# Kernel tuning notes

Hardware: AMD Instinct MI355X
Metric: run time of the kernel (lower is better)

## Reference

```python
import jax, jax.numpy as jnp
import numpy as np

LOG2E = 1.44269504


def setup_inputs() -> dict:
    key = jax.random.key(0)
    k1, k2, k3, k4 = jax.random.split(key, 4)
    B, Sq, Skv, Hq, Hkv, D = 2, 2048, 2048, 16, 4, 128
    q = jax.random.normal(k1, (B, Sq, Hq, D), dtype=jnp.float32)
    k = jax.random.normal(k2, (B, Skv, Hkv, D), dtype=jnp.float32)
    v = jax.random.normal(k3, (B, Skv, Hkv, D), dtype=jnp.float32)
    attn_mask = jax.random.normal(k4, (B, Hq, Sq, Skv), dtype=jnp.float32)
    return {"q": q, "k": k, "v": v, "attn_mask": attn_mask}


def reference(q, k, v, attn_mask):
    # q: [B, Sq, Hq, D]; k, v: [B, Skv, Hkv, D]; attn_mask: [B, Hq, Sq, Skv]
    B, Sq, Hq, D = q.shape
    Skv, Hkv = k.shape[1], k.shape[2]
    sm_scale = 1.0 / (D ** 0.5)

    qt = jnp.transpose(q, (0, 2, 1, 3))  # [B, Hq, Sq, D]
    kt = jnp.transpose(k, (0, 2, 1, 3))  # [B, Hkv, Skv, D]
    vt = jnp.transpose(v, (0, 2, 1, 3))  # [B, Hkv, Skv, D]

    # GQA head sharing: q-head h reads kv-head h % Hkv
    head_map = jnp.arange(Hq) % Hkv
    ke = kt[:, head_map]  # [B, Hq, Skv, D]
    ve = vt[:, head_map]  # [B, Hq, Skv, D]

    # scaled scores + additive mask (kernel: qk*sm_scale + attn_mask)
    logits = jnp.einsum('bhqd,bhkd->bhqk', qt, ke) * sm_scale + attn_mask

    # causal masking: kernel adds -1e6 in the log2 domain after LOG2E scaling
    s2 = logits * LOG2E
    causal_ok = jnp.arange(Sq)[:, None] >= jnp.arange(Skv)[None, :]
    s2 = s2 + jnp.where(causal_ok, 0.0, -1000000.0)

    # online-softmax equivalent: stable exp2 softmax along kv
    m = jnp.max(s2, axis=-1, keepdims=True)
    p = jnp.exp2(s2 - m)  # [B, Hq, Sq, Skv]
    l = jnp.sum(p, axis=-1, keepdims=True)
    o = jnp.einsum('bhqk,bhkd->bhqd', p, ve) / l

    return jnp.transpose(o, (0, 2, 1, 3))  # [B, Sq, Hq, D]
```

## Files before the change

kernel.cpp:

```cpp
#include <hip/hip_runtime.h>
#include <hip/hip_bf16.h>
#include <stdint.h>

static constexpr int B_   = 2;
static constexpr int SQ   = 2048;
static constexpr int SKV  = 2048;
static constexpr int HQ   = 16;
static constexpr int HKV  = 4;
static constexpr int DH   = 128;

static constexpr int BM = 64;
static constexpr int BN = 64;

static constexpr int KLD = DH + 8;
static constexpr int VLD = BN + 6;
static constexpr int PLD = BN + 4;

#define LOG2E 1.44269504f
static constexpr float SM_SCALE = 0.08838834764831845f;

static constexpr float SMAX = 24.0f;

typedef unsigned short ushort_t;
typedef __attribute__((ext_vector_type(8))) short bf16x8;
typedef __attribute__((ext_vector_type(4))) short bf16x4;
typedef __attribute__((ext_vector_type(4))) float f32x4;
typedef __attribute__((ext_vector_type(2))) unsigned int uint2v;

__device__ __forceinline__ ushort_t f2bf(float f) {
    union { __bf16 b; ushort_t u; } c;
    c.b = (__bf16)f;
    return c.u;
}
__device__ __forceinline__ unsigned int f2bf2(float lo, float hi) {
    return (unsigned int)f2bf(lo) | ((unsigned int)f2bf(hi) << 16);
}

extern "C" __global__ __launch_bounds__(256, 2)
void fa_fwd(const float* __restrict__ q, const float* __restrict__ k,
            const float* __restrict__ v, const float* __restrict__ mask,
            float* __restrict__ out)
{
    __shared__ __align__(16) ushort_t lK[BN * KLD];
    __shared__ __align__(16) ushort_t lV[DH * VLD];
    __shared__ __align__(16) float    lP[4 * 16 * PLD];

    const int bh   = blockIdx.x;
    const int h    = bh & 15;
    const int b    = bh >> 4;
    const int qblk = 31 - blockIdx.y;
    const int hk   = h & (HKV - 1);
    const int tid  = threadIdx.x;
    const int wave = tid >> 6;
    const int lane = tid & 63;
    const int lrow = lane & 15;
    const int quad = lane >> 4;
    const int q0   = qblk * BM;

    const size_t qbase = ((size_t)((b * SQ + q0 + wave * 16 + lrow) * HQ + h)) * DH;
    bf16x8 qf[4];
#pragma unroll
    for (int s = 0; s < 4; ++s) {
        const f32x4 a = *(const f32x4*)(q + qbase + s * 32 + quad * 8);
        const f32x4 c = *(const f32x4*)(q + qbase + s * 32 + quad * 8 + 4);
#pragma unroll
        for (int j = 0; j < 4; ++j) {
            qf[s][j]     = (short)f2bf(a[j]);
            qf[s][j + 4] = (short)f2bf(c[j]);
        }
    }

    f32x4 oacc[8];
#pragma unroll
    for (int i = 0; i < 8; ++i) oacc[i] = (f32x4){0.f, 0.f, 0.f, 0.f};
    float lsum[4] = {0.f, 0.f, 0.f, 0.f};

    float* lPw = lP + wave * 16 * PLD;

    const int krow = tid >> 5;
    const int kcol = (tid & 31) * 4;
    const size_t kgbase = ((size_t)((b * SKV + krow) * HKV + hk)) * DH + kcol;
    const int vd  = tid & 127;
    const int vkg = tid >> 7;
    const size_t vgbase = ((size_t)((b * SKV + vkg * 4) * HKV + hk)) * DH + vd;
    const float* mptr = mask
        + ((size_t)(b * HQ + h) * SQ + (q0 + wave * 16 + quad * 4)) * SKV + lrow;

    const int niter = qblk + 1;

    f32x4 kreg[8];
    float vreg[8][4];
    unsigned int kbh[8][2], vbh[8][2];
    float mv[4][4];

#define LOAD_KV(KV0) do {                                                        \
    _Pragma("unroll")                                                            \
    for (int i = 0; i < 8; ++i)                                                  \
        kreg[i] = *(const f32x4*)(k + kgbase + (size_t)((KV0) + 8 * i) * (HKV * DH)); \
    _Pragma("unroll")                                                            \
    for (int g = 0; g < 8; ++g) {                                                \
        const float* vp = v + vgbase + (size_t)((KV0) + 8 * g) * (HKV * DH);     \
        vreg[g][0] = vp[0];                                                      \
        vreg[g][1] = vp[HKV * DH];                                               \
        vreg[g][2] = vp[2 * HKV * DH];                                           \
        vreg[g][3] = vp[3 * HKV * DH];                                           \
    }                                                                            \
} while (0)

#define CONV_KV() do {                                                           \
    _Pragma("unroll")                                                            \
    for (int i = 0; i < 8; ++i) {                                                \
        kbh[i][0] = f2bf2(kreg[i][0], kreg[i][1]);                               \
        kbh[i][1] = f2bf2(kreg[i][2], kreg[i][3]);                               \
    }                                                                            \
    _Pragma("unroll")                                                            \
    for (int g = 0; g < 8; ++g) {                                                \
        vbh[g][0] = f2bf2(vreg[g][0], vreg[g][1]);                               \
        vbh[g][1] = f2bf2(vreg[g][2], vreg[g][3]);                               \
    }                                                                            \
} while (0)

    LOAD_KV(0);
#pragma unroll
    for (int r = 0; r < 4; ++r)
#pragma unroll
        for (int n = 0; n < 4; ++n)
            mv[r][n] = __builtin_nontemporal_load(mptr + (size_t)r * SKV + n * 16);
    CONV_KV();

    for (int it = 0; it < niter; ++it) {
        const int kv0 = it * BN;
        const bool last = (it + 1 == niter);

        __syncthreads();

#pragma unroll
        for (int i = 0; i < 8; ++i) {
            uint2v kw; kw[0] = kbh[i][0]; kw[1] = kbh[i][1];
            *(uint2v*)&lK[(krow + 8 * i) * KLD + kcol] = kw;
        }
#pragma unroll
        for (int g = 0; g < 8; ++g) {
            unsigned int* dst = (unsigned int*)&lV[vd * VLD + (vkg + 2 * g) * 4];
            dst[0] = vbh[g][0];
            dst[1] = vbh[g][1];
        }
        __syncthreads();

        if (!last) LOAD_KV(kv0 + BN);

        const bool diag = (kv0 == q0);

        f32x4 S[4];
#pragma unroll
        for (int n = 0; n < 4; ++n) {
            f32x4 acc = (f32x4){0.f, 0.f, 0.f, 0.f};
#pragma unroll
            for (int s = 0; s < 4; ++s) {
                const bf16x8 kf = *(const bf16x8*)&lK[(n * 16 + lrow) * KLD + s * 32 + quad * 8];
                acc = __builtin_amdgcn_mfma_f32_16x16x32_bf16(qf[s], kf, acc, 0, 0, 0);
            }
            S[n] = acc;
        }

#pragma unroll
        for (int r = 0; r < 4; ++r) {
            const int row = q0 + wave * 16 + quad * 4 + r;
            float ps = 0.f;
#pragma unroll
            for (int n = 0; n < 4; ++n) {
                const int col = n * 16 + lrow;
                float s2 = S[n][r] * (SM_SCALE * LOG2E) + (mv[r][n] * LOG2E - SMAX);
                if (diag && (kv0 + col > row)) s2 -= 1000000.0f;
                const float p = exp2f(s2);
                S[n][r] = p;
                ps += p;
            }
            lsum[r] += ps;
        }

        if (!last) {
#pragma unroll
            for (int r = 0; r < 4; ++r)
#pragma unroll
                for (int n = 0; n < 4; ++n)
                    mv[r][n] = __builtin_nontemporal_load(
                        mptr + (size_t)r * SKV + (kv0 + BN) + n * 16);
        }

#pragma unroll
        for (int r = 0; r < 4; ++r)
#pragma unroll
            for (int n = 0; n < 4; ++n)
                lPw[(quad * 4 + r) * PLD + n * 16 + lrow] = S[n][r];

        bf16x8 pfr[2];
#pragma unroll
        for (int s = 0; s < 2; ++s) {
            const float* pp = lPw + lrow * PLD + s * 32 + quad * 8;
            const f32x4 p0 = *(const f32x4*)(pp);
            const f32x4 p1 = *(const f32x4*)(pp + 4);
            union { bf16x8 v; unsigned int u[4]; } pf;
            pf.u[0] = f2bf2(p0[0], p0[1]);
            pf.u[1] = f2bf2(p0[2], p0[3]);
            pf.u[2] = f2bf2(p1[0], p1[1]);
            pf.u[3] = f2bf2(p1[2], p1[3]);
            pfr[s] = pf.v;
        }

#pragma unroll
        for (int o8 = 0; o8 < 8; ++o8) {
#pragma unroll
            for (int s = 0; s < 2; ++s) {
                const ushort_t* vp = &lV[(o8 * 16 + lrow) * VLD + s * 32 + quad * 8];
                union { bf16x8 v; unsigned int u[4]; } vf;
#pragma unroll
                for (int u2 = 0; u2 < 4; ++u2)
                    vf.u[u2] = *(const unsigned int*)(vp + 2 * u2);
                oacc[o8] = __builtin_amdgcn_mfma_f32_16x16x32_bf16(pfr[s], vf.v, oacc[o8], 0, 0, 0);
            }
        }

        if (!last) CONV_KV();
    }

    float rl[4];
#pragma unroll
    for (int r = 0; r < 4; ++r) {
        float s = lsum[r];
#pragma unroll
        for (int off = 1; off < 16; off <<= 1)
            s += __shfl_xor(s, off, 64);
        rl[r] = 1.0f / s;
    }
#pragma unroll
    for (int r = 0; r < 4; ++r) {
        const size_t ob = ((size_t)((b * SQ + q0 + wave * 16 + quad * 4 + r) * HQ + h)) * DH;
#pragma unroll
        for (int o8 = 0; o8 < 8; ++o8)
            out[ob + o8 * 16 + lrow] = oacc[o8][r] * rl[r];
    }
}

extern "C" void kernel_launch(void* const* d_in, const int* in_sizes, int n_in,
                              void* d_out, int out_size, void* d_ws, size_t ws_size,
                              hipStream_t stream)
{
    (void)in_sizes; (void)n_in; (void)out_size; (void)d_ws; (void)ws_size;
    const float* q = (const float*)d_in[0];
    const float* k = (const float*)d_in[1];
    const float* v = (const float*)d_in[2];
    const float* m = (const float*)d_in[3];
    float* o = (float*)d_out;
    dim3 grid(B_ * HQ, SQ / BM, 1);
    fa_fwd<<<grid, 256, 0, stream>>>(q, k, v, m, o);
}
```

Measured before the change: 739.5 us.

## Double-buffer K/V in LDS and store P as bf16

K and V tiles now live in two LDS buffers, so the next tile is converted and written during the current iteration, cutting the main loop from two barriers to one. The P staging buffer now holds bf16 instead of fp32, halving its LDS traffic and moving the conversion to the write side. LDS use rises by roughly one more K and V tile, which may limit occupancy at two blocks per CU.

Result: no change. 742.7 us (+0.4%).

```diff
diff --git a/kernel.cpp b/kernel.cpp
--- a/kernel.cpp
+++ b/kernel.cpp
@@ -14,7 +14,10 @@
 
 static constexpr int KLD = DH + 8;
 static constexpr int VLD = BN + 6;
-static constexpr int PLD = BN + 4;
+static constexpr int PLD = BN + 8;
+
+static constexpr int KBUF = BN * KLD;
+static constexpr int VBUF = DH * VLD;
 
 #define LOG2E 1.44269504f
 static constexpr float SM_SCALE = 0.08838834764831845f;
@@ -23,7 +26,6 @@
 
 typedef unsigned short ushort_t;
 typedef __attribute__((ext_vector_type(8))) short bf16x8;
-typedef __attribute__((ext_vector_type(4))) short bf16x4;
 typedef __attribute__((ext_vector_type(4))) float f32x4;
 typedef __attribute__((ext_vector_type(2))) unsigned int uint2v;
 
@@ -41,9 +43,9 @@
             const float* __restrict__ v, const float* __restrict__ mask,
             float* __restrict__ out)
 {
-    __shared__ __align__(16) ushort_t lK[BN * KLD];
-    __shared__ __align__(16) ushort_t lV[DH * VLD];
-    __shared__ __align__(16) float    lP[4 * 16 * PLD];
+    __shared__ __align__(16) ushort_t lK[2 * KBUF];
+    __shared__ __align__(16) ushort_t lV[2 * VBUF];
+    __shared__ __align__(16) ushort_t lP[4 * 16 * PLD];
 
     const int bh   = blockIdx.x;
     const int h    = bh & 15;
@@ -75,7 +77,7 @@
     for (int i = 0; i < 8; ++i) oacc[i] = (f32x4){0.f, 0.f, 0.f, 0.f};
     float lsum[4] = {0.f, 0.f, 0.f, 0.f};
 
-    float* lPw = lP + wave * 16 * PLD;
+    ushort_t* lPw = lP + wave * 16 * PLD;
 
     const int krow = tid >> 5;
     const int kcol = (tid & 31) * 4;
@@ -90,7 +92,6 @@
 
     f32x4 kreg[8];
     float vreg[8][4];
-    unsigned int kbh[8][2], vbh[8][2];
     float mv[4][4];
 
 #define LOAD_KV(KV0) do {                                                        \
@@ -107,16 +108,19 @@
     }                                                                            \
 } while (0)
 
-#define CONV_KV() do {                                                           \
+#define CONVWRITE(LKD, LVD) do {                                                 \
     _Pragma("unroll")                                                            \
     for (int i = 0; i < 8; ++i) {                                                \
-        kbh[i][0] = f2bf2(kreg[i][0], kreg[i][1]);                               \
-        kbh[i][1] = f2bf2(kreg[i][2], kreg[i][3]);                               \
+        uint2v kw;                                                               \
+        kw[0] = f2bf2(kreg[i][0], kreg[i][1]);                                   \
+        kw[1] = f2bf2(kreg[i][2], kreg[i][3]);                                   \
+        *(uint2v*)&(LKD)[(krow + 8 * i) * KLD + kcol] = kw;                      \
     }                                                                            \
     _Pragma("unroll")                                                            \
     for (int g = 0; g < 8; ++g) {                                                \
-        vbh[g][0] = f2bf2(vreg[g][0], vreg[g][1]);                               \
-        vbh[g][1] = f2bf2(vreg[g][2], vreg[g][3]);                               \
+        unsigned int* dst = (unsigned int*)&(LVD)[vd * VLD + (vkg + 2 * g) * 4]; \
+        dst[0] = f2bf2(vreg[g][0], vreg[g][1]);                                  \
+        dst[1] = f2bf2(vreg[g][2], vreg[g][3]);                                  \
     }                                                                            \
 } while (0)
 
@@ -126,28 +130,18 @@
 #pragma unroll
         for (int n = 0; n < 4; ++n)
             mv[r][n] = __builtin_nontemporal_load(mptr + (size_t)r * SKV + n * 16);
-    CONV_KV();
+    CONVWRITE(lK, lV);
+    __syncthreads();
 
     for (int it = 0; it < niter; ++it) {
         const int kv0 = it * BN;
-        const bool last = (it + 1 == niter);
-
-        __syncthreads();
-
-#pragma unroll
-        for (int i = 0; i < 8; ++i) {
-            uint2v kw; kw[0] = kbh[i][0]; kw[1] = kbh[i][1];
-            *(uint2v*)&lK[(krow + 8 * i) * KLD + kcol] = kw;
-        }
-#pragma unroll
-        for (int g = 0; g < 8; ++g) {
-            unsigned int* dst = (unsigned int*)&lV[vd * VLD + (vkg + 2 * g) * 4];
-            dst[0] = vbh[g][0];
-            dst[1] = vbh[g][1];
-        }
-        __syncthreads();
-
-        if (!last) LOAD_KV(kv0 + BN);
+        const int cur = it & 1;
+        const ushort_t* lKc = lK + cur * KBUF;
+        const ushort_t* lVc = lV + cur * VBUF;
+        ushort_t* lKn = lK + (cur ^ 1) * KBUF;
+        ushort_t* lVn = lV + (cur ^ 1) * VBUF;
+
+        if (it + 1 < niter) LOAD_KV(kv0 + BN);
 
         const bool diag = (kv0 == q0);
 
@@ -157,7 +151,7 @@
             f32x4 acc = (f32x4){0.f, 0.f, 0.f, 0.f};
 #pragma unroll
             for (int s = 0; s < 4; ++s) {
-                const bf16x8 kf = *(const bf16x8*)&lK[(n * 16 + lrow) * KLD + s * 32 + quad * 8];
+                const bf16x8 kf = *(const bf16x8*)&lKc[(n * 16 + lrow) * KLD + s * 32 + quad * 8];
                 acc = __builtin_amdgcn_mfma_f32_16x16x32_bf16(qf[s], kf, acc, 0, 0, 0);
             }
             S[n] = acc;
@@ -179,7 +173,7 @@
             lsum[r] += ps;
         }
 
-        if (!last) {
+        if (it + 1 < niter) {
 #pragma unroll
             for (int r = 0; r < 4; ++r)
 #pragma unroll
@@ -192,27 +186,18 @@
         for (int r = 0; r < 4; ++r)
 #pragma unroll
             for (int n = 0; n < 4; ++n)
-                lPw[(quad * 4 + r) * PLD + n * 16 + lrow] = S[n][r];
+                lPw[(quad * 4 + r) * PLD + n * 16 + lrow] = f2bf(S[n][r]);
 
         bf16x8 pfr[2];
 #pragma unroll
-        for (int s = 0; s < 2; ++s) {
-            const float* pp = lPw + lrow * PLD + s * 32 + quad * 8;
-            const f32x4 p0 = *(const f32x4*)(pp);
-            const f32x4 p1 = *(const f32x4*)(pp + 4);
-            union { bf16x8 v; unsigned int u[4]; } pf;
-            pf.u[0] = f2bf2(p0[0], p0[1]);
-            pf.u[1] = f2bf2(p0[2], p0[3]);
-            pf.u[2] = f2bf2(p1[0], p1[1]);
-            pf.u[3] = f2bf2(p1[2], p1[3]);
-            pfr[s] = pf.v;
-        }
+        for (int s = 0; s < 2; ++s)
+            pfr[s] = *(const bf16x8*)&lPw[lrow * PLD + s * 32 + quad * 8];
 
 #pragma unroll
         for (int o8 = 0; o8 < 8; ++o8) {
 #pragma unroll
             for (int s = 0; s < 2; ++s) {
-                const ushort_t* vp = &lV[(o8 * 16 + lrow) * VLD + s * 32 + quad * 8];
+                const ushort_t* vp = &lVc[(o8 * 16 + lrow) * VLD + s * 32 + quad * 8];
                 union { bf16x8 v; unsigned int u[4]; } vf;
 #pragma unroll
                 for (int u2 = 0; u2 < 4; ++u2)
@@ -221,7 +206,8 @@
             }
         }
 
-        if (!last) CONV_KV();
+        if (it + 1 < niter) CONVWRITE(lKn, lVn);
+        __syncthreads();
     }
 
     float rl[4];
```
